# Optimization experiments

Measured on AMD Instinct MI355X. Metric: run time of the kernel, lower is better.

## Reference

```python
import jax, jax.numpy as jnp
import numpy as np

N_WIRES = 8
N_QLAYERS = 1
DIM = 1 << N_WIRES  # 256

# bits[s, w] = w-th bit of basis state s; wire 0 is the MOST significant bit
# (torchquantum stores states as [bsz, 2, 2, ..., 2] with wire i at axis i+1)
_BITS = ((np.arange(DIM)[:, None] >> (N_WIRES - 1 - np.arange(N_WIRES))) & 1).astype(np.float32)


def setup_inputs() -> dict:
    key = jax.random.key(0)
    ks = jax.random.split(key, 5)
    pi = float(np.pi)
    return {
        "input_features": jax.random.normal(ks[0], (4, 4096, N_WIRES), jnp.float32),
        "params_ry1": jax.random.uniform(ks[1], (N_QLAYERS, N_WIRES), jnp.float32, -pi, pi),
        "params_crz1": jax.random.uniform(ks[2], (N_QLAYERS, N_WIRES), jnp.float32, -pi, pi),
        "params_ry2": jax.random.uniform(ks[3], (N_QLAYERS, N_WIRES), jnp.float32, -pi, pi),
        "params_crz2": jax.random.uniform(ks[4], (N_QLAYERS, N_WIRES), jnp.float32, -pi, pi),
    }


def _apply_ry(state, wire, theta):
    """Apply RY(theta) = [[c,-s],[s,c]] (c=cos(theta/2)) on `wire`.
    theta: scalar (shared param) or [B] (batched encoder angle)."""
    B = state.shape[0]
    c = jnp.cos(theta * 0.5)
    s = jnp.sin(theta * 0.5)
    if jnp.ndim(theta):  # per-batch angle
        c = c[:, None, None]
        s = s[:, None, None]
    st = state.reshape(B, 1 << wire, 2, -1)
    a, b = st[:, :, 0, :], st[:, :, 1, :]
    return jnp.stack([c * a - s * b, s * a + c * b], axis=2).reshape(B, DIM)


def _crz_block_diag(controls, targets, thetas, bits):
    """Fused diagonal of a commuting block of CRZ gates.
    CRZ(c,t,th) = diag over basis: 1 if bit_c==0 else exp(+/- i th/2) for bit_t=1/0.
    exponent contribution: bit_c * th * (bit_t - 0.5)."""
    expo = (bits[:, controls] * (bits[:, targets] - 0.5)) @ thetas  # [DIM]
    return jnp.exp(1j * expo).astype(jnp.complex64)


def _vqc_forward(x, params_ry1, params_crz1, params_ry2, params_crz2):
    B = x.shape[0]
    bits = jnp.asarray(_BITS)
    # |0...0>
    state = jnp.zeros((B, DIM), jnp.complex64).at[:, 0].set(1.0)

    idx = np.arange(N_WIRES)
    ctrl1, tgt1 = idx, (idx + 1) % N_WIRES  # crz block 1: wires [i, i+1]
    ctrl2, tgt2 = idx, (idx - 1) % N_WIRES  # crz block 2: wires [i, i-1]

    for k in range(N_QLAYERS):
        # tensor-product encoder: RY(x_i) on wire i
        for i in range(N_WIRES):
            state = _apply_ry(state, i, x[:, i])
        # CRZ ring (all diagonal -> fused)
        state = state * _crz_block_diag(ctrl1, tgt1, params_crz1[k], bits)[None, :]
        # trainable RY layer 1
        for i in range(N_WIRES):
            state = _apply_ry(state, i, params_ry1[k, i])
        # reverse CRZ ring (diagonal -> fused)
        state = state * _crz_block_diag(ctrl2, tgt2, params_crz2[k], bits)[None, :]
        # trainable RY layer 2
        for i in range(N_WIRES):
            state = _apply_ry(state, i, params_ry2[k, i])

    # PauliZ expectation on every wire: <Z_w> = sum_s |amp_s|^2 * (1 - 2*bit_w(s))
    probs = (state.real ** 2 + state.imag ** 2)  # [B, DIM]
    signs = 1.0 - 2.0 * bits                      # [DIM, N_WIRES]
    return probs @ signs                          # [B, N_WIRES]


def reference(input_features, params_ry1, params_crz1, params_ry2, params_crz2):
    bsz, slen, fz = input_features.shape
    x = input_features.reshape(-1, fz)
    out = _vqc_forward(x, params_ry1, params_crz1, params_ry2, params_crz2)
    return out.reshape(bsz, slen, fz)
```

## Files before the change

### kernel.cpp

```cpp
#include <hip/hip_runtime.h>
#include <math.h>

#define NW 8

template<int CTRL>
__device__ __forceinline__ float dpp_x(float v) {
    return __int_as_float(
        __builtin_amdgcn_update_dpp(0, __float_as_int(v), CTRL, 0xF, 0xF, true));
}
__device__ __forceinline__ float swz_xor4(float v) {
    return __int_as_float(__builtin_amdgcn_ds_swizzle(__float_as_int(v), 0x101F));
}
#define XCH1(v) dpp_x<0xB1>(v)
#define XCH2(v) dpp_x<0x4E>(v)
#define XCH8(v) dpp_x<0x128>(v)
#define XCH4(v) swz_xor4(v)

__global__ __launch_bounds__(256) void vqc_kernel(
    const float* __restrict__ x,
    const float* __restrict__ ry1,
    const float* __restrict__ crz1,
    const float* __restrict__ ry2,
    const float* __restrict__ crz2,
    float* __restrict__ out,
    int B)
{
    __shared__ __align__(16) float Tc1[320], Ts1[320], Tc2[320], Ts2[320];

    const int t = threadIdx.x;
    {
        const int n = t;
        float e1 = 0.f, e2 = 0.f;
#pragma unroll
        for (int i = 0; i < NW; ++i) {
            float bc  = (float)((n >> (7 - i)) & 1);
            float bt1 = (float)((n >> (7 - ((i + 1) & 7))) & 1);
            float bt2 = (float)((n >> (7 - ((i + 7) & 7))) & 1);
            e1 += bc * crz1[i] * (bt1 - 0.5f);
            e2 += bc * crz2[i] * (bt2 - 0.5f);
        }
        const int j  = n & 15;
        const int nh = n >> 4;
        const int sl = ((nh >> 3) & 1) | (((nh >> 2) & 1) << 1)
                     | ((nh & 1) << 2) | (((nh >> 1) & 1) << 3);
        const int idx = sl * 20 + j;
        float s, c;
        __sincosf(e1, &s, &c);  Tc1[idx] = c;  Ts1[idx] = s;
        __sincosf(e2, &s, &c);  Tc2[idx] = c;  Ts2[idx] = s;
    }
    __syncthreads();

    const int lane = t & 63;
    const int sl   = lane & 15;
    const int g    = lane >> 4;

    float rc1[8], rs1[8], rc2[8], rs2[8];
#pragma unroll
    for (int i = 0; i < 8; ++i) {
        __sincosf(0.5f * ry1[i], &rs1[i], &rc1[i]);
        __sincosf(0.5f * ry2[i], &rs2[i], &rc2[i]);
    }

    const float* pc1 = &Tc1[sl * 20];
    const float* ps1 = &Ts1[sl * 20];
    const float* pc2 = &Tc2[sl * 20];
    const float* ps2 = &Ts2[sl * 20];

    const int wavesPerBlock = blockDim.x >> 6;
    const int gwave = blockIdx.x * wavesPerBlock + (t >> 6);
    const int TW = gridDim.x * wavesPerBlock;

#define CROSS_WIRE(RC, RS, WI, SLBIT, EXCH)                                 \
    { float c = RC[WI], s = RS[WI];                                         \
      float se = (sl & SLBIT) ? s : -s;                                     \
      _Pragma("unroll")                                                     \
      for (int j = 0; j < 16; ++j) {                                        \
          float pre = EXCH(re[j]);                                          \
          float pim = EXCH(im[j]);                                          \
          re[j] = fmaf(se, pre, c * re[j]);                                 \
          im[j] = fmaf(se, pim, c * im[j]);                                 \
      } }

#define INLANE_WIRE(RC, RS, WI, M)                                          \
    { float c = RC[WI], s = RS[WI];                                         \
      _Pragma("unroll")                                                     \
      for (int j = 0; j < 16; ++j) if (!(j & M)) {                          \
          int hi = j | M;                                                   \
          float rl = re[j], rh = re[hi], il = im[j], ih = im[hi];           \
          re[j]  = c * rl - s * rh;  re[hi] = fmaf(s, rl, c * rh);          \
          im[j]  = c * il - s * ih;  im[hi] = fmaf(s, il, c * ih);          \
      } }

#define RY_LAYER(RC, RS)                                                    \
    do {                                                                    \
        CROSS_WIRE(RC, RS, 0, 1, XCH1);                                     \
        CROSS_WIRE(RC, RS, 1, 2, XCH2);                                     \
        CROSS_WIRE(RC, RS, 2, 8, XCH8);                                     \
        CROSS_WIRE(RC, RS, 3, 4, XCH4);                                     \
        INLANE_WIRE(RC, RS, 4, 8);                                          \
        INLANE_WIRE(RC, RS, 5, 4);                                          \
        INLANE_WIRE(RC, RS, 6, 2);                                          \
        INLANE_WIRE(RC, RS, 7, 1);                                          \
    } while (0)

    for (int b0 = gwave * 4; b0 < B; b0 += TW * 4) {
        const int b  = b0 + g;
        const int bl = (b < B) ? b : (B - 1);

        const float4* xp = (const float4*)(x + (size_t)bl * NW);
        float4 xa = xp[0], xb = xp[1];
        float cs[8], sn[8];
        __sincosf(0.5f * xa.x, &sn[0], &cs[0]);
        __sincosf(0.5f * xa.y, &sn[1], &cs[1]);
        __sincosf(0.5f * xa.z, &sn[2], &cs[2]);
        __sincosf(0.5f * xa.w, &sn[3], &cs[3]);
        __sincosf(0.5f * xb.x, &sn[4], &cs[4]);
        __sincosf(0.5f * xb.y, &sn[5], &cs[5]);
        __sincosf(0.5f * xb.z, &sn[6], &cs[6]);
        __sincosf(0.5f * xb.w, &sn[7], &cs[7]);

        float pcf = ((sl & 1) ? sn[0] : cs[0])
                  * ((sl & 2) ? sn[1] : cs[1])
                  * ((sl & 8) ? sn[2] : cs[2])
                  * ((sl & 4) ? sn[3] : cs[3]);

        float a[16];
#pragma unroll
        for (int j = 0; j < 16; ++j) {
            float f = ((j & 1) ? sn[7] : cs[7]);
            f *= ((j & 2) ? sn[6] : cs[6]);
            f *= ((j & 4) ? sn[5] : cs[5]);
            f *= ((j & 8) ? sn[4] : cs[4]);
            a[j] = pcf * f;
        }

        float re[16], im[16];
#pragma unroll
        for (int q = 0; q < 4; ++q) {
            float4 cq = *(const float4*)&pc1[4 * q];
            float4 sq = *(const float4*)&ps1[4 * q];
            re[4*q+0] = a[4*q+0] * cq.x;  im[4*q+0] = a[4*q+0] * sq.x;
            re[4*q+1] = a[4*q+1] * cq.y;  im[4*q+1] = a[4*q+1] * sq.y;
            re[4*q+2] = a[4*q+2] * cq.z;  im[4*q+2] = a[4*q+2] * sq.z;
            re[4*q+3] = a[4*q+3] * cq.w;  im[4*q+3] = a[4*q+3] * sq.w;
        }

        RY_LAYER(rc1, rs1);

#pragma unroll
        for (int q = 0; q < 4; ++q) {
            float4 cq = *(const float4*)&pc2[4 * q];
            float4 sq = *(const float4*)&ps2[4 * q];
            float nr, ni;
            nr = re[4*q+0]*cq.x - im[4*q+0]*sq.x; ni = re[4*q+0]*sq.x + im[4*q+0]*cq.x; re[4*q+0] = nr; im[4*q+0] = ni;
            nr = re[4*q+1]*cq.y - im[4*q+1]*sq.y; ni = re[4*q+1]*sq.y + im[4*q+1]*cq.y; re[4*q+1] = nr; im[4*q+1] = ni;
            nr = re[4*q+2]*cq.z - im[4*q+2]*sq.z; ni = re[4*q+2]*sq.z + im[4*q+2]*cq.z; re[4*q+2] = nr; im[4*q+2] = ni;
            nr = re[4*q+3]*cq.w - im[4*q+3]*sq.w; ni = re[4*q+3]*sq.w + im[4*q+3]*cq.w; re[4*q+3] = nr; im[4*q+3] = ni;
        }

        RY_LAYER(rc2, rs2);

        float p[16];
#pragma unroll
        for (int j = 0; j < 16; ++j) p[j] = re[j]*re[j] + im[j]*im[j];

        float s2_[8], v7 = 0.f;
#pragma unroll
        for (int k = 0; k < 8; ++k) { s2_[k] = p[2*k] + p[2*k+1]; v7 += p[2*k] - p[2*k+1]; }
        float s4_[4], v6 = 0.f;
#pragma unroll
        for (int k = 0; k < 4; ++k) { s4_[k] = s2_[2*k] + s2_[2*k+1]; v6 += s2_[2*k] - s2_[2*k+1]; }
        float s8a = s4_[0] + s4_[1], s8b = s4_[2] + s4_[3];
        float v5 = (s4_[0] - s4_[1]) + (s4_[2] - s4_[3]);
        float v4 = s8a - s8b;
        float v0 = s8a + s8b;

#define BFLY_R(EXCH, M)                                                     \
        { float o0 = EXCH(v0), o4 = EXCH(v4), o5 = EXCH(v5),                \
                o6 = EXCH(v6), o7 = EXCH(v7);                               \
          if (sl & M) { v0 = o0 - v0; v4 = o4 - v4; v5 = o5 - v5;           \
                        v6 = o6 - v6; v7 = o7 - v7; }                       \
          else        { v0 = o0 + v0; v4 = o4 + v4; v5 = o5 + v5;           \
                        v6 = o6 + v6; v7 = o7 + v7; } }
        BFLY_R(XCH1, 1);
        BFLY_R(XCH2, 2);
        BFLY_R(XCH4, 4);
        BFLY_R(XCH8, 8);
#undef BFLY_R

        if (b < B) {
            float* ob = out + (size_t)b * NW;
            if      (sl == 1) ob[0] = v0;
            else if (sl == 2) ob[1] = v0;
            else if (sl == 8) ob[2] = v0;
            else if (sl == 4) ob[3] = v0;
            else if (sl == 0) *(float4*)(ob + 4) = make_float4(v4, v5, v6, v7);
        }
    }
#undef RY_LAYER
#undef CROSS_WIRE
#undef INLANE_WIRE
}

extern "C" void kernel_launch(void* const* d_in, const int* in_sizes, int n_in,
                              void* d_out, int out_size, void* d_ws, size_t ws_size,
                              hipStream_t stream) {
    const float* x    = (const float*)d_in[0];
    const float* ry1  = (const float*)d_in[1];
    const float* crz1 = (const float*)d_in[2];
    const float* ry2  = (const float*)d_in[3];
    const float* crz2 = (const float*)d_in[4];
    float* out = (float*)d_out;

    int B = in_sizes[0] / NW;
    int blocks = (B + 15) / 16;
    if (blocks < 1) blocks = 1;
    vqc_kernel<<<blocks, 256, 0, stream>>>(x, ry1, crz1, ry2, crz2, out, B);
}
```

Baseline: 71.38 us.

## Map each state to 8 lanes with 32 amplitudes per lane, drop swizzle exchange

Each statevector now spans 8 lanes holding 32 amplitudes each, instead of 16 lanes holding 16. Wire 3 becomes an in-lane rotation, so the ds_swizzle cross-lane exchange and one butterfly reduction stage go away. Each wave now handles 8 batch elements, the grid-stride loop is removed and the launch uses half as many blocks. This doubles register pressure per thread (64 floats of state), which the launch_bounds occupancy hint of 2 is meant to accommodate, at the risk of spills or lower occupancy.

```diff
diff --git a/kernel.cpp b/kernel.cpp
--- a/kernel.cpp
+++ b/kernel.cpp
@@ -8,15 +8,11 @@
     return __int_as_float(
         __builtin_amdgcn_update_dpp(0, __float_as_int(v), CTRL, 0xF, 0xF, true));
 }
-__device__ __forceinline__ float swz_xor4(float v) {
-    return __int_as_float(__builtin_amdgcn_ds_swizzle(__float_as_int(v), 0x101F));
-}
 #define XCH1(v) dpp_x<0xB1>(v)
 #define XCH2(v) dpp_x<0x4E>(v)
 #define XCH8(v) dpp_x<0x128>(v)
-#define XCH4(v) swz_xor4(v)
-
-__global__ __launch_bounds__(256) void vqc_kernel(
+
+__global__ __launch_bounds__(256, 2) void vqc_kernel(
     const float* __restrict__ x,
     const float* __restrict__ ry1,
     const float* __restrict__ crz1,
@@ -25,7 +21,7 @@
     float* __restrict__ out,
     int B)
 {
-    __shared__ __align__(16) float Tc1[320], Ts1[320], Tc2[320], Ts2[320];
+    __shared__ __align__(16) float Tc1[288], Ts1[288], Tc2[288], Ts2[288];
 
     const int t = threadIdx.x;
     {
@@ -39,11 +35,9 @@
             e1 += bc * crz1[i] * (bt1 - 0.5f);
             e2 += bc * crz2[i] * (bt2 - 0.5f);
         }
-        const int j  = n & 15;
-        const int nh = n >> 4;
-        const int sl = ((nh >> 3) & 1) | (((nh >> 2) & 1) << 1)
-                     | ((nh & 1) << 2) | (((nh >> 1) & 1) << 3);
-        const int idx = sl * 20 + j;
+        const int j = n & 31;
+        const int u = (((n >> 7) & 1) << 2) | (((n >> 6) & 1) << 1) | ((n >> 5) & 1);
+        const int idx = u * 36 + j;
         float s, c;
         __sincosf(e1, &s, &c);  Tc1[idx] = c;  Ts1[idx] = s;
         __sincosf(e2, &s, &c);  Tc2[idx] = c;  Ts2[idx] = s;
@@ -51,8 +45,8 @@
     __syncthreads();
 
     const int lane = t & 63;
-    const int sl   = lane & 15;
-    const int g    = lane >> 4;
+    const int u = ((lane & 1) << 2) | (((lane >> 1) & 1) << 1) | ((lane >> 3) & 1);
+    const int g = ((lane >> 3) & 6) | ((lane >> 2) & 1);
 
     float rc1[8], rs1[8], rc2[8], rs2[8];
 #pragma unroll
@@ -61,20 +55,60 @@
         __sincosf(0.5f * ry2[i], &rs2[i], &rc2[i]);
     }
 
-    const float* pc1 = &Tc1[sl * 20];
-    const float* ps1 = &Ts1[sl * 20];
-    const float* pc2 = &Tc2[sl * 20];
-    const float* ps2 = &Ts2[sl * 20];
+    const float* pc1 = &Tc1[u * 36];
+    const float* ps1 = &Ts1[u * 36];
+    const float* pc2 = &Tc2[u * 36];
+    const float* ps2 = &Ts2[u * 36];
 
     const int wavesPerBlock = blockDim.x >> 6;
     const int gwave = blockIdx.x * wavesPerBlock + (t >> 6);
-    const int TW = gridDim.x * wavesPerBlock;
-
-#define CROSS_WIRE(RC, RS, WI, SLBIT, EXCH)                                 \
+
+    const int b  = gwave * 8 + g;
+    const int bl = (b < B) ? b : (B - 1);
+
+    const float4* xp = (const float4*)(x + (size_t)bl * NW);
+    float4 xa = xp[0], xb = xp[1];
+    float cs[8], sn[8];
+    __sincosf(0.5f * xa.x, &sn[0], &cs[0]);
+    __sincosf(0.5f * xa.y, &sn[1], &cs[1]);
+    __sincosf(0.5f * xa.z, &sn[2], &cs[2]);
+    __sincosf(0.5f * xa.w, &sn[3], &cs[3]);
+    __sincosf(0.5f * xb.x, &sn[4], &cs[4]);
+    __sincosf(0.5f * xb.y, &sn[5], &cs[5]);
+    __sincosf(0.5f * xb.z, &sn[6], &cs[6]);
+    __sincosf(0.5f * xb.w, &sn[7], &cs[7]);
+
+    float pcf = ((lane & 1) ? sn[0] : cs[0])
+              * ((lane & 2) ? sn[1] : cs[1])
+              * ((lane & 8) ? sn[2] : cs[2]);
+
+    float t2[2], t4[4], t8[8], t16[16], a[32];
+    t2[0] = pcf * cs[3];  t2[1] = pcf * sn[3];
+#pragma unroll
+    for (int k = 0; k < 2; ++k)  { t4[2*k]  = t2[k]  * cs[4];  t4[2*k+1]  = t2[k]  * sn[4]; }
+#pragma unroll
+    for (int k = 0; k < 4; ++k)  { t8[2*k]  = t4[k]  * cs[5];  t8[2*k+1]  = t4[k]  * sn[5]; }
+#pragma unroll
+    for (int k = 0; k < 8; ++k)  { t16[2*k] = t8[k]  * cs[6];  t16[2*k+1] = t8[k]  * sn[6]; }
+#pragma unroll
+    for (int k = 0; k < 16; ++k) { a[2*k]   = t16[k] * cs[7];  a[2*k+1]   = t16[k] * sn[7]; }
+
+    float re[32], im[32];
+#pragma unroll
+    for (int q = 0; q < 8; ++q) {
+        float4 cq = *(const float4*)&pc1[4 * q];
+        float4 sq = *(const float4*)&ps1[4 * q];
+        re[4*q+0] = a[4*q+0] * cq.x;  im[4*q+0] = a[4*q+0] * sq.x;
+        re[4*q+1] = a[4*q+1] * cq.y;  im[4*q+1] = a[4*q+1] * sq.y;
+        re[4*q+2] = a[4*q+2] * cq.z;  im[4*q+2] = a[4*q+2] * sq.z;
+        re[4*q+3] = a[4*q+3] * cq.w;  im[4*q+3] = a[4*q+3] * sq.w;
+    }
+
+#define CROSS_WIRE(RC, RS, WI, LBIT, EXCH)                                  \
     { float c = RC[WI], s = RS[WI];                                         \
-      float se = (sl & SLBIT) ? s : -s;                                     \
+      float se = (lane & LBIT) ? s : -s;                                    \
       _Pragma("unroll")                                                     \
-      for (int j = 0; j < 16; ++j) {                                        \
+      for (int j = 0; j < 32; ++j) {                                        \
           float pre = EXCH(re[j]);                                          \
           float pim = EXCH(im[j]);                                          \
           re[j] = fmaf(se, pre, c * re[j]);                                 \
@@ -84,7 +118,7 @@
 #define INLANE_WIRE(RC, RS, WI, M)                                          \
     { float c = RC[WI], s = RS[WI];                                         \
       _Pragma("unroll")                                                     \
-      for (int j = 0; j < 16; ++j) if (!(j & M)) {                          \
+      for (int j = 0; j < 32; ++j) if (!(j & M)) {                          \
           int hi = j | M;                                                   \
           float rl = re[j], rh = re[hi], il = im[j], ih = im[hi];           \
           re[j]  = c * rl - s * rh;  re[hi] = fmaf(s, rl, c * rh);          \
@@ -96,106 +130,65 @@
         CROSS_WIRE(RC, RS, 0, 1, XCH1);                                     \
         CROSS_WIRE(RC, RS, 1, 2, XCH2);                                     \
         CROSS_WIRE(RC, RS, 2, 8, XCH8);                                     \
-        CROSS_WIRE(RC, RS, 3, 4, XCH4);                                     \
+        INLANE_WIRE(RC, RS, 3, 16);                                         \
         INLANE_WIRE(RC, RS, 4, 8);                                          \
         INLANE_WIRE(RC, RS, 5, 4);                                          \
         INLANE_WIRE(RC, RS, 6, 2);                                          \
         INLANE_WIRE(RC, RS, 7, 1);                                          \
     } while (0)
 
-    for (int b0 = gwave * 4; b0 < B; b0 += TW * 4) {
-        const int b  = b0 + g;
-        const int bl = (b < B) ? b : (B - 1);
-
-        const float4* xp = (const float4*)(x + (size_t)bl * NW);
-        float4 xa = xp[0], xb = xp[1];
-        float cs[8], sn[8];
-        __sincosf(0.5f * xa.x, &sn[0], &cs[0]);
-        __sincosf(0.5f * xa.y, &sn[1], &cs[1]);
-        __sincosf(0.5f * xa.z, &sn[2], &cs[2]);
-        __sincosf(0.5f * xa.w, &sn[3], &cs[3]);
-        __sincosf(0.5f * xb.x, &sn[4], &cs[4]);
-        __sincosf(0.5f * xb.y, &sn[5], &cs[5]);
-        __sincosf(0.5f * xb.z, &sn[6], &cs[6]);
-        __sincosf(0.5f * xb.w, &sn[7], &cs[7]);
-
-        float pcf = ((sl & 1) ? sn[0] : cs[0])
-                  * ((sl & 2) ? sn[1] : cs[1])
-                  * ((sl & 8) ? sn[2] : cs[2])
-                  * ((sl & 4) ? sn[3] : cs[3]);
-
-        float a[16];
-#pragma unroll
-        for (int j = 0; j < 16; ++j) {
-            float f = ((j & 1) ? sn[7] : cs[7]);
-            f *= ((j & 2) ? sn[6] : cs[6]);
-            f *= ((j & 4) ? sn[5] : cs[5]);
-            f *= ((j & 8) ? sn[4] : cs[4]);
-            a[j] = pcf * f;
-        }
-
-        float re[16], im[16];
-#pragma unroll
-        for (int q = 0; q < 4; ++q) {
-            float4 cq = *(const float4*)&pc1[4 * q];
-            float4 sq = *(const float4*)&ps1[4 * q];
-            re[4*q+0] = a[4*q+0] * cq.x;  im[4*q+0] = a[4*q+0] * sq.x;
-            re[4*q+1] = a[4*q+1] * cq.y;  im[4*q+1] = a[4*q+1] * sq.y;
-            re[4*q+2] = a[4*q+2] * cq.z;  im[4*q+2] = a[4*q+2] * sq.z;
-            re[4*q+3] = a[4*q+3] * cq.w;  im[4*q+3] = a[4*q+3] * sq.w;
-        }
-
-        RY_LAYER(rc1, rs1);
-
-#pragma unroll
-        for (int q = 0; q < 4; ++q) {
-            float4 cq = *(const float4*)&pc2[4 * q];
-            float4 sq = *(const float4*)&ps2[4 * q];
-            float nr, ni;
-            nr = re[4*q+0]*cq.x - im[4*q+0]*sq.x; ni = re[4*q+0]*sq.x + im[4*q+0]*cq.x; re[4*q+0] = nr; im[4*q+0] = ni;
-            nr = re[4*q+1]*cq.y - im[4*q+1]*sq.y; ni = re[4*q+1]*sq.y + im[4*q+1]*cq.y; re[4*q+1] = nr; im[4*q+1] = ni;
-            nr = re[4*q+2]*cq.z - im[4*q+2]*sq.z; ni = re[4*q+2]*sq.z + im[4*q+2]*cq.z; re[4*q+2] = nr; im[4*q+2] = ni;
-            nr = re[4*q+3]*cq.w - im[4*q+3]*sq.w; ni = re[4*q+3]*sq.w + im[4*q+3]*cq.w; re[4*q+3] = nr; im[4*q+3] = ni;
-        }
-
-        RY_LAYER(rc2, rs2);
-
-        float p[16];
-#pragma unroll
-        for (int j = 0; j < 16; ++j) p[j] = re[j]*re[j] + im[j]*im[j];
-
-        float s2_[8], v7 = 0.f;
-#pragma unroll
-        for (int k = 0; k < 8; ++k) { s2_[k] = p[2*k] + p[2*k+1]; v7 += p[2*k] - p[2*k+1]; }
-        float s4_[4], v6 = 0.f;
-#pragma unroll
-        for (int k = 0; k < 4; ++k) { s4_[k] = s2_[2*k] + s2_[2*k+1]; v6 += s2_[2*k] - s2_[2*k+1]; }
-        float s8a = s4_[0] + s4_[1], s8b = s4_[2] + s4_[3];
-        float v5 = (s4_[0] - s4_[1]) + (s4_[2] - s4_[3]);
-        float v4 = s8a - s8b;
-        float v0 = s8a + s8b;
+    RY_LAYER(rc1, rs1);
+
+#pragma unroll
+    for (int q = 0; q < 8; ++q) {
+        float4 cq = *(const float4*)&pc2[4 * q];
+        float4 sq = *(const float4*)&ps2[4 * q];
+        float nr, ni;
+        nr = re[4*q+0]*cq.x - im[4*q+0]*sq.x; ni = re[4*q+0]*sq.x + im[4*q+0]*cq.x; re[4*q+0] = nr; im[4*q+0] = ni;
+        nr = re[4*q+1]*cq.y - im[4*q+1]*sq.y; ni = re[4*q+1]*sq.y + im[4*q+1]*cq.y; re[4*q+1] = nr; im[4*q+1] = ni;
+        nr = re[4*q+2]*cq.z - im[4*q+2]*sq.z; ni = re[4*q+2]*sq.z + im[4*q+2]*cq.z; re[4*q+2] = nr; im[4*q+2] = ni;
+        nr = re[4*q+3]*cq.w - im[4*q+3]*sq.w; ni = re[4*q+3]*sq.w + im[4*q+3]*cq.w; re[4*q+3] = nr; im[4*q+3] = ni;
+    }
+
+    RY_LAYER(rc2, rs2);
+
+    float p[32];
+#pragma unroll
+    for (int j = 0; j < 32; ++j) p[j] = re[j]*re[j] + im[j]*im[j];
+
+    float s2_[16], d7 = 0.f;
+#pragma unroll
+    for (int k = 0; k < 16; ++k) { s2_[k] = p[2*k] + p[2*k+1]; d7 += p[2*k] - p[2*k+1]; }
+    float s4_[8], d6 = 0.f;
+#pragma unroll
+    for (int k = 0; k < 8; ++k)  { s4_[k] = s2_[2*k] + s2_[2*k+1]; d6 += s2_[2*k] - s2_[2*k+1]; }
+    float s8_[4], d5 = 0.f;
+#pragma unroll
+    for (int k = 0; k < 4; ++k)  { s8_[k] = s4_[2*k] + s4_[2*k+1]; d5 += s4_[2*k] - s4_[2*k+1]; }
+    float s16a = s8_[0] + s8_[1], s16b = s8_[2] + s8_[3];
+    float d4 = (s8_[0] - s8_[1]) + (s8_[2] - s8_[3]);
+    float d3 = s16a - s16b;
+    float v0 = s16a + s16b;
 
 #define BFLY_R(EXCH, M)                                                     \
-        { float o0 = EXCH(v0), o4 = EXCH(v4), o5 = EXCH(v5),                \
-                o6 = EXCH(v6), o7 = EXCH(v7);                               \
-          if (sl & M) { v0 = o0 - v0; v4 = o4 - v4; v5 = o5 - v5;           \
-                        v6 = o6 - v6; v7 = o7 - v7; }                       \
-          else        { v0 = o0 + v0; v4 = o4 + v4; v5 = o5 + v5;           \
-                        v6 = o6 + v6; v7 = o7 + v7; } }
-        BFLY_R(XCH1, 1);
-        BFLY_R(XCH2, 2);
-        BFLY_R(XCH4, 4);
-        BFLY_R(XCH8, 8);
+    { float o0 = EXCH(v0), o3 = EXCH(d3), o4 = EXCH(d4),                    \
+            o5 = EXCH(d5), o6 = EXCH(d6), o7 = EXCH(d7);                    \
+      if (lane & M) { v0 = o0 - v0; d3 = o3 - d3; d4 = o4 - d4;             \
+                      d5 = o5 - d5; d6 = o6 - d6; d7 = o7 - d7; }           \
+      else          { v0 = o0 + v0; d3 = o3 + d3; d4 = o4 + d4;             \
+                      d5 = o5 + d5; d6 = o6 + d6; d7 = o7 + d7; } }
+    BFLY_R(XCH1, 1);
+    BFLY_R(XCH2, 2);
+    BFLY_R(XCH8, 8);
 #undef BFLY_R
 
-        if (b < B) {
-            float* ob = out + (size_t)b * NW;
-            if      (sl == 1) ob[0] = v0;
-            else if (sl == 2) ob[1] = v0;
-            else if (sl == 8) ob[2] = v0;
-            else if (sl == 4) ob[3] = v0;
-            else if (sl == 0) *(float4*)(ob + 4) = make_float4(v4, v5, v6, v7);
-        }
+    if (b < B) {
+        const int loc = lane & 11;
+        float* ob = out + (size_t)b * NW;
+        if      (loc == 0) { ob[3] = d3; *(float4*)(ob + 4) = make_float4(d4, d5, d6, d7); }
+        else if (loc == 1) ob[0] = v0;
+        else if (loc == 2) ob[1] = v0;
+        else if (loc == 8) ob[2] = v0;
     }
 #undef RY_LAYER
 #undef CROSS_WIRE
@@ -213,7 +206,7 @@
     float* out = (float*)d_out;
 
     int B = in_sizes[0] / NW;
-    int blocks = (B + 15) / 16;
+    int blocks = (B + 31) / 32;
     if (blocks < 1) blocks = 1;
     vqc_kernel<<<blocks, 256, 0, stream>>>(x, ry1, crz1, ry2, crz2, out, B);
 }
```

New measurement: 69.79 us. 2.2% less time.
